# Performance work log

Measured on AMD Instinct MI355X. Metric: run time of the kernel, lower is better.

The kernel has to match this reference:

```python
import jax, jax.numpy as jnp
import numpy as np

TEMPERATURE = 0.07
NEG = -1e9  # stand-in for -inf on the diagonal; exp(NEG) == 0


def setup_inputs() -> dict:
    key = jax.random.key(0)
    k1, k2, k3 = jax.random.split(key, 3)
    B, D = 4096, 1024
    return {
        "anchor_features": jax.random.normal(k1, (B, D), dtype=jnp.float32),
        "positive_features": jax.random.normal(k2, (B, D), dtype=jnp.float32),
        "labels": jax.random.randint(k3, (B,), 0, 2),
    }


def reference(anchor_features, positive_features, labels):
    B = anchor_features.shape[0]
    # L2-normalize (normalize=True)
    a = anchor_features / jnp.linalg.norm(anchor_features, axis=1, keepdims=True)
    p = positive_features / jnp.linalg.norm(positive_features, axis=1, keepdims=True)
    feats = jnp.concatenate([a, p], axis=0)                      # [2B, D]
    sim = jnp.matmul(feats, feats.T) / TEMPERATURE               # [2B, 2B]
    diag = jnp.eye(2 * B, dtype=bool)
    sim = jnp.where(diag, NEG, sim)                              # mask self-similarity
    # logsumexp over all non-self entries per row (diag contributes exp(NEG)=0)
    lse = jax.nn.logsumexp(sim, axis=1)                          # [2B]
    # positive pair similarity: sim[i, i+B] == sim[i+B, i] == <a_i, p_i>/t
    cross = jnp.sum(a * p, axis=1) / TEMPERATURE                 # [B]
    pos_sim = jnp.concatenate([cross, cross])                    # [2B]
    lab = jnp.concatenate([labels, labels]).astype(sim.dtype)    # [2B], 0/1
    per_row = (-pos_sim + lse) * lab
    num_pos = jnp.sum(lab)
    return jnp.where(num_pos > 0, jnp.sum(per_row) / num_pos, jnp.float32(0.0))
```

## Files before the change

kernel.cpp:

```cpp
#include <hip/hip_runtime.h>
#include <hip/hip_bf16.h>

#define TEMP_INV (1.0f / 0.07f)
#define LOG2E 1.4426950408889634f
#define LN2 0.6931471805599453f
#define CFIX 21.0f

typedef __attribute__((ext_vector_type(4))) float f32x4;

__device__ __forceinline__ void gload16(const unsigned char* g,
                                        unsigned char* l) {
  __builtin_amdgcn_global_load_lds(
      (const __attribute__((address_space(1))) void*)g,
      (__attribute__((address_space(3))) void*)l, 16, 0, 0);
}

__global__ __launch_bounds__(256) void norm_kernel(
    const float* __restrict__ A, const float* __restrict__ P,
    unsigned char* __restrict__ F, float* __restrict__ cross,
    float* __restrict__ lsum, int B, int D) {
  const int row = blockIdx.x;
  const int t = threadIdx.x;
  {
    const int zi = row * 256 + t;
    if (zi < 2 * B) lsum[zi] = 0.f;
  }
  const float4* a4 = reinterpret_cast<const float4*>(A + (size_t)row * D);
  const float4* p4 = reinterpret_cast<const float4*>(P + (size_t)row * D);
  const int n4 = D >> 2;
  float sa = 0.f, sp = 0.f, sx = 0.f;
  for (int i = t; i < n4; i += 256) {
    float4 av = a4[i], pv = p4[i];
    sa += av.x * av.x + av.y * av.y + av.z * av.z + av.w * av.w;
    sp += pv.x * pv.x + pv.y * pv.y + pv.z * pv.z + pv.w * pv.w;
    sx += av.x * pv.x + av.y * pv.y + av.z * pv.z + av.w * pv.w;
  }
#pragma unroll
  for (int off = 32; off; off >>= 1) {
    sa += __shfl_down(sa, off);
    sp += __shfl_down(sp, off);
    sx += __shfl_down(sx, off);
  }
  __shared__ float red[3][4];
  const int wid = t >> 6, lane = t & 63;
  if (lane == 0) { red[0][wid] = sa; red[1][wid] = sp; red[2][wid] = sx; }
  __syncthreads();
  sa = red[0][0] + red[0][1] + red[0][2] + red[0][3];
  sp = red[1][0] + red[1][1] + red[1][2] + red[1][3];
  sx = red[2][0] + red[2][1] + red[2][2] + red[2][3];
  const float ian = rsqrtf(sa), ipn = rsqrtf(sp);
  const float ia = ian * 16.f, ip = ipn * 16.f;
  unsigned char* fa = F + (size_t)row * D;
  unsigned char* fp = F + (size_t)(B + row) * D;
  for (int i = t; i < n4; i += 256) {
    float4 av = a4[i], pv = p4[i];
    int qa = 0, qp = 0;
    qa = __builtin_amdgcn_cvt_pk_fp8_f32(av.x * ia, av.y * ia, qa, false);
    qa = __builtin_amdgcn_cvt_pk_fp8_f32(av.z * ia, av.w * ia, qa, true);
    qp = __builtin_amdgcn_cvt_pk_fp8_f32(pv.x * ip, pv.y * ip, qp, false);
    qp = __builtin_amdgcn_cvt_pk_fp8_f32(pv.z * ip, pv.w * ip, qp, true);
    reinterpret_cast<int*>(fa)[i] = qa;
    reinterpret_cast<int*>(fp)[i] = qp;
  }
  if (t == 0) cross[row] = sx * ian * ipn;
}

template <int MFN>
__device__ __forceinline__ void gram_body(
    unsigned char* LDS, const unsigned char* F, float* lsum, int D,
    int r0, int c0, bool diag) {
  const int t = threadIdx.x;
  const int lane = t & 63, w = t >> 6;
  const int lo = lane & 15, hi = lane >> 4;
  const int wr = w >> 2, wn = w & 3;

  const int ciA = t & (MFN * 64 - 1);
  const int lrA = ciA >> 3, cuA = (ciA & 7) ^ (lrA & 7);
  const int trA = lrA * 4 + (cuA >> 1), kcA = (cuA & 1) << 4;
  const int lrB = t >> 3, cuB = (t & 7) ^ (lrB & 7);
  const int trB = lrB * 4 + (cuB >> 1), kcB = (cuB & 1) << 4;
  const unsigned char* sA = F + (size_t)(c0 + trA) * D + kcA;
  const unsigned char* sB = F + (size_t)(r0 + trB) * D + kcB;
  const int dstA = (w % MFN) * 1024;
  const int dstB = w * 1024;

  int offA[MFN], offB[4];
#pragma unroll
  for (int mf = 0; mf < MFN; ++mf) {
    const int r = wr * (MFN * 16) + mf * 16 + lo;
    const int lr = r >> 2;
    const int cu = ((r & 3) << 1) | (hi >> 1);
    offA[mf] = lr * 128 + ((cu ^ (lr & 7)) << 4) + ((hi & 1) << 3);
  }
#pragma unroll
  for (int nf = 0; nf < 4; ++nf) {
    const int r = wn * 64 + nf * 16 + lo;
    const int lr = r >> 2;
    const int cu = ((r & 3) << 1) | (hi >> 1);
    offB[nf] = lr * 128 + ((cu ^ (lr & 7)) << 4) + ((hi & 1) << 3);
  }

#define STAGE(V, KS)                                                       \
  do {                                                                    \
    int v_ = (V); if (v_ > 15) v_ = 15;                                   \
    const int o_ = v_ * 64 + (KS) * 32;                                   \
    gload16(sA + o_, LDS + ((V) & 3) * 32768 + (KS) * 8192 + dstA);       \
    gload16(sB + o_, LDS + ((V) & 3) * 32768 + 16384 + (KS) * 8192 + dstB); \
  } while (0)

  f32x4 acc[MFN][4];
#pragma unroll
  for (int a = 0; a < MFN; ++a)
#pragma unroll
    for (int bb = 0; bb < 4; ++bb) acc[a][bb] = (f32x4){0.f, 0.f, 0.f, 0.f};

  STAGE(0, 0); STAGE(0, 1);
  STAGE(1, 0); STAGE(1, 1);
  STAGE(2, 0); STAGE(2, 1);

  for (int v = 0; v < 16; ++v) {
    const int buf = v & 3;
    asm volatile("s_waitcnt vmcnt(8)" ::: "memory");
    __builtin_amdgcn_s_barrier();
    asm volatile("" ::: "memory");

    const unsigned char* RA0 = LDS + buf * 32768;
    const unsigned char* RA1 = RA0 + 8192;
    const unsigned char* RB0 = LDS + buf * 32768 + 16384;
    const unsigned char* RB1 = RB0 + 8192;
    long a0[MFN], a1[MFN], b0[4], b1[4];
#pragma unroll
    for (int nf = 0; nf < 4; ++nf) b0[nf] = *(const long*)(RB0 + offB[nf]);
#pragma unroll
    for (int mf = 0; mf < MFN; ++mf) a0[mf] = *(const long*)(RA0 + offA[mf]);
#pragma unroll
    for (int nf = 0; nf < 4; ++nf) b1[nf] = *(const long*)(RB1 + offB[nf]);
#pragma unroll
    for (int mf = 0; mf < MFN; ++mf) a1[mf] = *(const long*)(RA1 + offA[mf]);

    STAGE(v + 3, 0);
    STAGE(v + 3, 1);

    __builtin_amdgcn_s_setprio(1);
#pragma unroll
    for (int mf = 0; mf < MFN; ++mf)
#pragma unroll
      for (int nf = 0; nf < 4; ++nf)
        acc[mf][nf] = __builtin_amdgcn_mfma_f32_16x16x32_fp8_fp8(
            a0[mf], b0[nf], acc[mf][nf], 0, 0, 0);
#pragma unroll
    for (int mf = 0; mf < MFN; ++mf)
#pragma unroll
      for (int nf = 0; nf < 4; ++nf)
        acc[mf][nf] = __builtin_amdgcn_mfma_f32_16x16x32_fp8_fp8(
            a1[mf], b1[nf], acc[mf][nf], 0, 0, 0);
    __builtin_amdgcn_s_setprio(0);
    asm volatile("" ::: "memory");
  }

  const float scl = LOG2E * TEMP_INV / 256.f;
  float s_i[4] = {0.f, 0.f, 0.f, 0.f};
  float s_j[MFN * 4];
#pragma unroll
  for (int q = 0; q < MFN * 4; ++q) s_j[q] = 0.f;
  {
    const int jb2 = c0 + wr * (MFN * 16);
#pragma unroll
    for (int nf = 0; nf < 4; ++nf) {
      const int dg = (r0 + wn * 64 + nf * 16 + lo) - jb2;
#pragma unroll
      for (int mf = 0; mf < MFN; ++mf)
#pragma unroll
        for (int rg = 0; rg < 4; ++rg) {
          const int jloc = mf * 16 + hi * 4 + rg;
          float e = exp2f(acc[mf][nf][rg] * scl - CFIX);
          if (diag && dg == jloc) e = 0.f;
          s_i[nf] += e;
          s_j[mf * 4 + rg] += e;
        }
    }
  }
#pragma unroll
  for (int nf = 0; nf < 4; ++nf) {
    float v = s_i[nf];
    v += __shfl_xor(v, 16);
    v += __shfl_xor(v, 32);
    if (hi == 0) atomicAdd(&lsum[r0 + wn * 64 + nf * 16 + lo], v);
  }
  if (!diag) {
#pragma unroll
    for (int q = 0; q < MFN * 4; ++q) {
      float v = s_j[q];
      v += __shfl_xor(v, 1);
      v += __shfl_xor(v, 2);
      v += __shfl_xor(v, 4);
      v += __shfl_xor(v, 8);
      if (lo == 0)
        atomicAdd(&lsum[c0 + wr * (MFN * 16) + (q >> 2) * 16 + hi * 4 +
                        (q & 3)],
                  v);
    }
  }
  asm volatile("s_waitcnt vmcnt(0)" ::: "memory");
#undef STAGE
}

__global__ __launch_bounds__(512, 2) void gram_lse_kernel(
    const unsigned char* __restrict__ F, float* __restrict__ lsum, int NN,
    int D) {
  __shared__ unsigned char lds8[4][2][2][8192];
  const int nrb = NN >> 8;
  const int ntri = nrb * (nrb + 1) / 2;
  const int nfull = ntri - 16;
  const int bidx = blockIdx.x;
  int lin, c0extra = 0;
  bool half = false;
  if (bidx < nfull) {
    lin = bidx;
    if ((nfull & 7) == 0) lin = (bidx & 7) * (nfull >> 3) + (bidx >> 3);
  } else {
    const int idx = bidx - nfull;
    lin = nfull + (idx >> 1);
    c0extra = (idx & 1) * 128;
    half = true;
  }
  int by = (int)((sqrtf(8.f * (float)lin + 1.f) - 1.f) * 0.5f);
  while ((by + 1) * (by + 2) / 2 <= lin) ++by;
  while (by * (by + 1) / 2 > lin) --by;
  const int bx = lin - by * (by + 1) / 2;
  const int r0 = bx * 256;
  const int c0 = by * 256 + c0extra;
  const bool diag = (bx == by);

  if (!half)
    gram_body<8>(&lds8[0][0][0][0], F, lsum, D, r0, c0, diag);
  else
    gram_body<4>(&lds8[0][0][0][0], F, lsum, D, r0, c0, diag);
}

__global__ __launch_bounds__(256) void finalize_part(
    const float* __restrict__ lsum, const float* __restrict__ cross,
    const int* __restrict__ labels, float* __restrict__ bsum,
    float* __restrict__ bcnt, int B) {
  const int NN = 2 * B;
  const int i = blockIdx.x * 256 + threadIdx.x;
  float sum = 0.f, cnt = 0.f;
  if (i < NN) {
    const float lse = LN2 * (CFIX + log2f(lsum[i]));
    const float lab = (float)labels[i % B];
    sum = (lse - cross[i % B] * TEMP_INV) * lab;
    cnt = lab;
  }
#pragma unroll
  for (int off = 32; off; off >>= 1) {
    sum += __shfl_down(sum, off);
    cnt += __shfl_down(cnt, off);
  }
  __shared__ float rs[4], rc[4];
  const int wid = threadIdx.x >> 6, lane = threadIdx.x & 63;
  if (lane == 0) { rs[wid] = sum; rc[wid] = cnt; }
  __syncthreads();
  if (threadIdx.x == 0) {
    bsum[blockIdx.x] = rs[0] + rs[1] + rs[2] + rs[3];
    bcnt[blockIdx.x] = rc[0] + rc[1] + rc[2] + rc[3];
  }
}

__global__ __launch_bounds__(64) void finalize_final(
    const float* __restrict__ bsum, const float* __restrict__ bcnt,
    float* __restrict__ out, int nb) {
  const int t = threadIdx.x;
  float s = (t < nb) ? bsum[t] : 0.f;
  float c = (t < nb) ? bcnt[t] : 0.f;
#pragma unroll
  for (int off = 32; off; off >>= 1) {
    s += __shfl_down(s, off);
    c += __shfl_down(c, off);
  }
  if (t == 0) out[0] = (c > 0.f) ? s / c : 0.f;
}

extern "C" void kernel_launch(void* const* d_in, const int* in_sizes, int n_in,
                              void* d_out, int out_size, void* d_ws, size_t ws_size,
                              hipStream_t stream) {
  const float* A = (const float*)d_in[0];
  const float* P = (const float*)d_in[1];
  const int* labels = (const int*)d_in[2];
  float* out = (float*)d_out;
  const int B = in_sizes[2];
  const int D = in_sizes[0] / B;
  const int NN = 2 * B;

  char* ws = (char*)d_ws;
  unsigned char* F = (unsigned char*)ws;
  size_t off = (size_t)NN * D;
  off = (off + 255) & ~(size_t)255;
  float* cross = (float*)(ws + off);
  off += (size_t)B * sizeof(float);
  off = (off + 255) & ~(size_t)255;
  float* lsum = (float*)(ws + off);
  off += (size_t)NN * sizeof(float);
  off = (off + 255) & ~(size_t)255;
  float* bsum = (float*)(ws + off);
  off += 64 * sizeof(float);
  float* bcnt = (float*)(ws + off);

  norm_kernel<<<B, 256, 0, stream>>>(A, P, F, cross, lsum, B, D);
  const int nrb = NN >> 8;
  const int ntri = nrb * (nrb + 1) / 2;
  const int nblk = (ntri - 16) + 32;
  gram_lse_kernel<<<nblk, 512, 0, stream>>>(F, lsum, NN, D);
  const int nb = (NN + 255) / 256;
  finalize_part<<<nb, 256, 0, stream>>>(lsum, cross, labels, bsum, bcnt, B);
  finalize_final<<<1, 64, 0, stream>>>(bsum, bcnt, out, nb);
}
```

Baseline: 116.1 us.

## Restructure full-tile gram loop into fine-grained 8-phase double-buffered pipeline

```diff
diff --git a/kernel.cpp b/kernel.cpp
--- a/kernel.cpp
+++ b/kernel.cpp
@@ -65,10 +65,156 @@
   if (t == 0) cross[row] = sx * ian * ipn;
 }
 
-template <int MFN>
-__device__ __forceinline__ void gram_body(
+
+__device__ __forceinline__ void gram_full8(
     unsigned char* LDS, const unsigned char* F, float* lsum, int D,
     int r0, int c0, bool diag) {
+  const int t = threadIdx.x;
+  const int lane = t & 63, w = t >> 6;
+  const int lo = lane & 15, hi = lane >> 4;
+  const int wr = w >> 2, wn = w & 3;
+
+  const int lineS = t >> 3, cS = (t & 7) ^ (lineS & 7);
+  const int trS = lineS * 4 + (cS >> 1), kcS = (cS & 1) << 4;
+  const unsigned char* sA = F + (size_t)(c0 + trS) * D + kcS;
+  const unsigned char* sB = F + (size_t)(r0 + trS) * D + kcS;
+  const int dstW = w * 1024;
+
+  int offA[8], offB[4];
+#pragma unroll
+  for (int mf = 0; mf < 8; ++mf) {
+    const int r = wr * 128 + mf * 16 + lo;
+    const int lr = r >> 2;
+    const int cu = ((r & 3) << 1) | (hi >> 1);
+    offA[mf] = lr * 128 + ((cu ^ (lr & 7)) << 4) + ((hi & 1) << 3);
+  }
+#pragma unroll
+  for (int nf = 0; nf < 4; ++nf) {
+    const int r = wn * 64 + nf * 16 + lo;
+    const int lr = r >> 2;
+    const int cu = ((r & 3) << 1) | (hi >> 1);
+    offB[nf] = lr * 128 + ((cu ^ (lr & 7)) << 4) + ((hi & 1) << 3);
+  }
+
+#define STAGE_A(T, KS, BUF)                                                 \
+  do {                                                                      \
+    int v_ = (T); if (v_ > 15) v_ = 15;                                     \
+    gload16(sA + v_ * 64 + (KS) * 32,                                       \
+            LDS + (BUF) * 32768 + (KS) * 8192 + dstW);                      \
+  } while (0)
+#define STAGE_B(T, KS, BUF)                                                 \
+  do {                                                                      \
+    int v_ = (T); if (v_ > 15) v_ = 15;                                     \
+    gload16(sB + v_ * 64 + (KS) * 32,                                       \
+            LDS + (BUF) * 32768 + 16384 + (KS) * 8192 + dstW);              \
+  } while (0)
+
+  f32x4 acc[8][4];
+  long bfr[4];
+
+#define PHASE(BUF, MH, KS, READB, STAGE_STMT, WAIT2)                          \
+  do {                                                                        \
+    const unsigned char* RA_ = LDS + (BUF) * 32768 + (KS) * 8192;             \
+    const unsigned char* RB_ = RA_ + 16384;                                   \
+    if (READB) {                                                              \
+      _Pragma("unroll") for (int nf = 0; nf < 4; ++nf)                        \
+          bfr[nf] = *(const long*)(RB_ + offB[nf]);                           \
+    }                                                                         \
+    long af[4];                                                               \
+    _Pragma("unroll") for (int m = 0; m < 4; ++m)                             \
+        af[m] = *(const long*)(RA_ + offA[(MH)*4 + m]);                       \
+    STAGE_STMT;                                                               \
+    if (WAIT2) asm volatile("s_waitcnt vmcnt(2)" ::: "memory");               \
+    asm volatile("" ::: "memory");                                            \
+    __builtin_amdgcn_s_barrier();                                             \
+    asm volatile("" ::: "memory");                                            \
+    __builtin_amdgcn_s_setprio(1);                                            \
+    _Pragma("unroll") for (int m = 0; m < 4; ++m)                             \
+      _Pragma("unroll") for (int nf = 0; nf < 4; ++nf)                        \
+          acc[(MH)*4 + m][nf] = __builtin_amdgcn_mfma_f32_16x16x32_fp8_fp8(   \
+              af[m], bfr[nf], acc[(MH)*4 + m][nf], 0, 0, 0);                  \
+    __builtin_amdgcn_s_setprio(0);                                            \
+    asm volatile("" ::: "memory");                                            \
+    __builtin_amdgcn_s_barrier();                                             \
+    asm volatile("" ::: "memory");                                            \
+  } while (0)
+
+#pragma unroll
+  for (int a = 0; a < 8; ++a)
+#pragma unroll
+    for (int bb = 0; bb < 4; ++bb) acc[a][bb] = (f32x4){0.f, 0.f, 0.f, 0.f};
+
+  STAGE_A(0, 0, 0); STAGE_B(0, 0, 0);
+  STAGE_A(0, 1, 0); STAGE_B(0, 1, 0);
+  STAGE_A(1, 0, 1); STAGE_B(1, 0, 1);
+  STAGE_B(1, 1, 1);
+  asm volatile("s_waitcnt vmcnt(3)" ::: "memory");
+  __builtin_amdgcn_s_barrier();
+  asm volatile("" ::: "memory");
+
+  for (int it = 0; it < 8; ++it) {
+    const int tt = it * 2;
+    PHASE(0, 0, 0, true,  STAGE_A(tt + 1, 1, 1), false);
+    PHASE(0, 1, 0, false, STAGE_B(tt + 2, 0, 0), false);
+    PHASE(0, 0, 1, true,  STAGE_A(tt + 2, 0, 0), false);
+    PHASE(0, 1, 1, false, STAGE_B(tt + 2, 1, 0), true);
+    PHASE(1, 0, 0, true,  STAGE_A(tt + 2, 1, 0), false);
+    PHASE(1, 1, 0, false, STAGE_B(tt + 3, 0, 1), false);
+    PHASE(1, 0, 1, true,  STAGE_A(tt + 3, 0, 1), false);
+    PHASE(1, 1, 1, false, STAGE_B(tt + 3, 1, 1), true);
+  }
+
+  const float scl = LOG2E * TEMP_INV / 256.f;
+  float s_i[4] = {0.f, 0.f, 0.f, 0.f};
+  float s_j[32];
+#pragma unroll
+  for (int q = 0; q < 32; ++q) s_j[q] = 0.f;
+  {
+    const int jb2 = c0 + wr * 128;
+#pragma unroll
+    for (int nf = 0; nf < 4; ++nf) {
+      const int dg = (r0 + wn * 64 + nf * 16 + lo) - jb2;
+#pragma unroll
+      for (int mf = 0; mf < 8; ++mf)
+#pragma unroll
+        for (int rg = 0; rg < 4; ++rg) {
+          const int jloc = mf * 16 + hi * 4 + rg;
+          float e = exp2f(acc[mf][nf][rg] * scl - CFIX);
+          if (diag && dg == jloc) e = 0.f;
+          s_i[nf] += e;
+          s_j[mf * 4 + rg] += e;
+        }
+    }
+  }
+#pragma unroll
+  for (int nf = 0; nf < 4; ++nf) {
+    float v = s_i[nf];
+    v += __shfl_xor(v, 16);
+    v += __shfl_xor(v, 32);
+    if (hi == 0) atomicAdd(&lsum[r0 + wn * 64 + nf * 16 + lo], v);
+  }
+  if (!diag) {
+#pragma unroll
+    for (int q = 0; q < 32; ++q) {
+      float v = s_j[q];
+      v += __shfl_xor(v, 1);
+      v += __shfl_xor(v, 2);
+      v += __shfl_xor(v, 4);
+      v += __shfl_xor(v, 8);
+      if (lo == 0)
+        atomicAdd(&lsum[c0 + wr * 128 + (q >> 2) * 16 + hi * 4 + (q & 3)], v);
+    }
+  }
+  asm volatile("s_waitcnt vmcnt(0)" ::: "memory");
+#undef PHASE
+#undef STAGE_A
+#undef STAGE_B
+}
+
+__device__ __forceinline__ void gram_half(
+    unsigned char* LDS, const unsigned char* F, float* lsum, int D,
+    int r0, int c0, bool diag) {
+  const int MFN = 4;
   const int t = threadIdx.x;
   const int lane = t & 63, w = t >> 6;
   const int lo = lane & 15, hi = lane >> 4;
@@ -100,11 +246,11 @@
     offB[nf] = lr * 128 + ((cu ^ (lr & 7)) << 4) + ((hi & 1) << 3);
   }
 
-#define STAGE(V, KS)                                                       \
-  do {                                                                    \
-    int v_ = (V); if (v_ > 15) v_ = 15;                                   \
-    const int o_ = v_ * 64 + (KS) * 32;                                   \
-    gload16(sA + o_, LDS + ((V) & 3) * 32768 + (KS) * 8192 + dstA);       \
+#define STAGE(V, KS)                                                        \
+  do {                                                                      \
+    int v_ = (V); if (v_ > 15) v_ = 15;                                     \
+    const int o_ = v_ * 64 + (KS) * 32;                                     \
+    gload16(sA + o_, LDS + ((V) & 3) * 32768 + (KS) * 8192 + dstA);         \
     gload16(sB + o_, LDS + ((V) & 3) * 32768 + 16384 + (KS) * 8192 + dstB); \
   } while (0)
 
@@ -126,7 +272,7 @@
 
     const unsigned char* RA0 = LDS + buf * 32768;
     const unsigned char* RA1 = RA0 + 8192;
-    const unsigned char* RB0 = LDS + buf * 32768 + 16384;
+    const unsigned char* RB0 = RA0 + 16384;
     const unsigned char* RB1 = RB0 + 8192;
     long a0[MFN], a1[MFN], b0[4], b1[4];
 #pragma unroll
@@ -208,7 +354,7 @@
 __global__ __launch_bounds__(512, 2) void gram_lse_kernel(
     const unsigned char* __restrict__ F, float* __restrict__ lsum, int NN,
     int D) {
-  __shared__ unsigned char lds8[4][2][2][8192];
+  __shared__ unsigned char lds8[4][32768];
   const int nrb = NN >> 8;
   const int ntri = nrb * (nrb + 1) / 2;
   const int nfull = ntri - 16;
@@ -233,9 +379,9 @@
   const bool diag = (bx == by);
 
   if (!half)
-    gram_body<8>(&lds8[0][0][0][0], F, lsum, D, r0, c0, diag);
+    gram_full8(&lds8[0][0], F, lsum, D, r0, c0, diag);
   else
-    gram_body<4>(&lds8[0][0][0][0], F, lsum, D, r0, c0, diag);
+    gram_half(&lds8[0][0], F, lsum, D, r0, c0, diag);
 }
 
 __global__ __launch_bounds__(256) void finalize_part(
```

Result: no change. 115.8 us (-0.2%).

## Split gram kernel into 1024-thread full-tile kernel and separate half-tile kernel

Applied to the files above, without the earlier changes.

```diff
diff --git a/kernel.cpp b/kernel.cpp
--- a/kernel.cpp
+++ b/kernel.cpp
@@ -65,10 +65,162 @@
   if (t == 0) cross[row] = sx * ian * ipn;
 }
 
-template <int MFN>
-__device__ __forceinline__ void gram_body(
-    unsigned char* LDS, const unsigned char* F, float* lsum, int D,
-    int r0, int c0, bool diag) {
+
+__global__ __launch_bounds__(1024) void gram_full_kernel(
+    const unsigned char* __restrict__ F, float* __restrict__ lsum, int NN,
+    int D) {
+  __shared__ unsigned char lds8[4][2][2][8192];
+  int lin = blockIdx.x;
+  lin = (lin & 7) * 64 + (lin >> 3);
+  int by = (int)((sqrtf(8.f * (float)lin + 1.f) - 1.f) * 0.5f);
+  while ((by + 1) * (by + 2) / 2 <= lin) ++by;
+  while (by * (by + 1) / 2 > lin) --by;
+  const int bx = lin - by * (by + 1) / 2;
+  const int r0 = bx * 256;
+  const int c0 = by * 256;
+  const bool diag = (bx == by);
+
+  const int t = threadIdx.x;
+  const int lane = t & 63, w = t >> 6;
+  const int lo = lane & 15, hi = lane >> 4;
+  const int wr = w >> 2, wn = w & 3;
+
+  const int KSa = t >> 9;
+  const int cS = t & 511;
+  const int lineS = cS >> 3, pS = (cS & 7) ^ (lineS & 7);
+  const int trS = lineS * 4 + (pS >> 1);
+  const int kcS = ((pS & 1) << 4) + KSa * 32;
+  const unsigned char* sA = F + (size_t)(c0 + trS) * D + kcS;
+  const unsigned char* sB = F + (size_t)(r0 + trS) * D + kcS;
+  const int dstW = (w & 7) * 1024;
+
+  int offA[4], offB[4];
+#pragma unroll
+  for (int mf = 0; mf < 4; ++mf) {
+    const int r = wr * 64 + mf * 16 + lo;
+    const int lr = r >> 2;
+    const int cu = ((r & 3) << 1) | (hi >> 1);
+    offA[mf] = lr * 128 + ((cu ^ (lr & 7)) << 4) + ((hi & 1) << 3);
+  }
+#pragma unroll
+  for (int nf = 0; nf < 4; ++nf) {
+    const int r = wn * 64 + nf * 16 + lo;
+    const int lr = r >> 2;
+    const int cu = ((r & 3) << 1) | (hi >> 1);
+    offB[nf] = lr * 128 + ((cu ^ (lr & 7)) << 4) + ((hi & 1) << 3);
+  }
+
+#define STAGE(V)                                                      \
+  do {                                                                \
+    int v_ = (V); if (v_ > 15) v_ = 15;                               \
+    gload16(sA + v_ * 64, &lds8[(V) & 3][0][KSa][dstW]);              \
+    gload16(sB + v_ * 64, &lds8[(V) & 3][1][KSa][dstW]);              \
+  } while (0)
+
+  f32x4 acc[4][4];
+#pragma unroll
+  for (int a = 0; a < 4; ++a)
+#pragma unroll
+    for (int bb = 0; bb < 4; ++bb) acc[a][bb] = (f32x4){0.f, 0.f, 0.f, 0.f};
+
+  STAGE(0); STAGE(1); STAGE(2);
+
+  for (int v = 0; v < 16; ++v) {
+    const int buf = v & 3;
+    asm volatile("s_waitcnt vmcnt(4)" ::: "memory");
+    __builtin_amdgcn_s_barrier();
+    asm volatile("" ::: "memory");
+
+    long a0[4], a1[4], b0[4], b1[4];
+#pragma unroll
+    for (int q = 0; q < 4; ++q) {
+      b0[q] = *(const long*)(&lds8[buf][1][0][0] + offB[q]);
+      a0[q] = *(const long*)(&lds8[buf][0][0][0] + offA[q]);
+      b1[q] = *(const long*)(&lds8[buf][1][1][0] + offB[q]);
+      a1[q] = *(const long*)(&lds8[buf][0][1][0] + offA[q]);
+    }
+
+    STAGE(v + 3);
+
+    __builtin_amdgcn_s_setprio(1);
+#pragma unroll
+    for (int mf = 0; mf < 4; ++mf)
+#pragma unroll
+      for (int nf = 0; nf < 4; ++nf)
+        acc[mf][nf] = __builtin_amdgcn_mfma_f32_16x16x32_fp8_fp8(
+            a0[mf], b0[nf], acc[mf][nf], 0, 0, 0);
+#pragma unroll
+    for (int mf = 0; mf < 4; ++mf)
+#pragma unroll
+      for (int nf = 0; nf < 4; ++nf)
+        acc[mf][nf] = __builtin_amdgcn_mfma_f32_16x16x32_fp8_fp8(
+            a1[mf], b1[nf], acc[mf][nf], 0, 0, 0);
+    __builtin_amdgcn_s_setprio(0);
+    asm volatile("" ::: "memory");
+  }
+
+  const float scl = LOG2E * TEMP_INV / 256.f;
+  float s_i[4] = {0.f, 0.f, 0.f, 0.f};
+  float s_j[16];
+#pragma unroll
+  for (int q = 0; q < 16; ++q) s_j[q] = 0.f;
+  {
+    const int dgb = (r0 + wn * 64) - (c0 + wr * 64);
+#pragma unroll
+    for (int nf = 0; nf < 4; ++nf) {
+      const int dg = dgb + nf * 16 + lo;
+#pragma unroll
+      for (int mf = 0; mf < 4; ++mf)
+#pragma unroll
+        for (int rg = 0; rg < 4; ++rg) {
+          const int jloc = mf * 16 + hi * 4 + rg;
+          float e = exp2f(acc[mf][nf][rg] * scl - CFIX);
+          if (diag && dg == jloc) e = 0.f;
+          s_i[nf] += e;
+          s_j[mf * 4 + rg] += e;
+        }
+    }
+  }
+#pragma unroll
+  for (int nf = 0; nf < 4; ++nf) {
+    float v = s_i[nf];
+    v += __shfl_xor(v, 16);
+    v += __shfl_xor(v, 32);
+    if (hi == 0) atomicAdd(&lsum[r0 + wn * 64 + nf * 16 + lo], v);
+  }
+  if (!diag) {
+#pragma unroll
+    for (int q = 0; q < 16; ++q) {
+      float v = s_j[q];
+      v += __shfl_xor(v, 1);
+      v += __shfl_xor(v, 2);
+      v += __shfl_xor(v, 4);
+      v += __shfl_xor(v, 8);
+      if (lo == 0)
+        atomicAdd(&lsum[c0 + wr * 64 + (q >> 2) * 16 + hi * 4 + (q & 3)], v);
+    }
+  }
+  asm volatile("s_waitcnt vmcnt(0)" ::: "memory");
+#undef STAGE
+}
+
+__global__ __launch_bounds__(512, 2) void gram_half_kernel(
+    const unsigned char* __restrict__ F, float* __restrict__ lsum, int NN,
+    int D) {
+  __shared__ unsigned char LDSb[4][32768];
+  unsigned char* LDS = &LDSb[0][0];
+  const int MFN = 4;
+  const int idx = blockIdx.x;
+  const int lin = 512 + (idx >> 1);
+  const int c0extra = (idx & 1) * 128;
+  int by = (int)((sqrtf(8.f * (float)lin + 1.f) - 1.f) * 0.5f);
+  while ((by + 1) * (by + 2) / 2 <= lin) ++by;
+  while (by * (by + 1) / 2 > lin) --by;
+  const int bx = lin - by * (by + 1) / 2;
+  const int r0 = bx * 256;
+  const int c0 = by * 256 + c0extra;
+  const bool diag = (bx == by);
+
   const int t = threadIdx.x;
   const int lane = t & 63, w = t >> 6;
   const int lo = lane & 15, hi = lane >> 4;
@@ -100,11 +252,11 @@
     offB[nf] = lr * 128 + ((cu ^ (lr & 7)) << 4) + ((hi & 1) << 3);
   }
 
-#define STAGE(V, KS)                                                       \
-  do {                                                                    \
-    int v_ = (V); if (v_ > 15) v_ = 15;                                   \
-    const int o_ = v_ * 64 + (KS) * 32;                                   \
-    gload16(sA + o_, LDS + ((V) & 3) * 32768 + (KS) * 8192 + dstA);       \
+#define STAGE(V, KS)                                                        \
+  do {                                                                      \
+    int v_ = (V); if (v_ > 15) v_ = 15;                                     \
+    const int o_ = v_ * 64 + (KS) * 32;                                     \
+    gload16(sA + o_, LDS + ((V) & 3) * 32768 + (KS) * 8192 + dstA);         \
     gload16(sB + o_, LDS + ((V) & 3) * 32768 + 16384 + (KS) * 8192 + dstB); \
   } while (0)
 
@@ -126,7 +278,7 @@
 
     const unsigned char* RA0 = LDS + buf * 32768;
     const unsigned char* RA1 = RA0 + 8192;
-    const unsigned char* RB0 = LDS + buf * 32768 + 16384;
+    const unsigned char* RB0 = RA0 + 16384;
     const unsigned char* RB1 = RB0 + 8192;
     long a0[MFN], a1[MFN], b0[4], b1[4];
 #pragma unroll
@@ -203,39 +355,6 @@
   }
   asm volatile("s_waitcnt vmcnt(0)" ::: "memory");
 #undef STAGE
-}
-
-__global__ __launch_bounds__(512, 2) void gram_lse_kernel(
-    const unsigned char* __restrict__ F, float* __restrict__ lsum, int NN,
-    int D) {
-  __shared__ unsigned char lds8[4][2][2][8192];
-  const int nrb = NN >> 8;
-  const int ntri = nrb * (nrb + 1) / 2;
-  const int nfull = ntri - 16;
-  const int bidx = blockIdx.x;
-  int lin, c0extra = 0;
-  bool half = false;
-  if (bidx < nfull) {
-    lin = bidx;
-    if ((nfull & 7) == 0) lin = (bidx & 7) * (nfull >> 3) + (bidx >> 3);
-  } else {
-    const int idx = bidx - nfull;
-    lin = nfull + (idx >> 1);
-    c0extra = (idx & 1) * 128;
-    half = true;
-  }
-  int by = (int)((sqrtf(8.f * (float)lin + 1.f) - 1.f) * 0.5f);
-  while ((by + 1) * (by + 2) / 2 <= lin) ++by;
-  while (by * (by + 1) / 2 > lin) --by;
-  const int bx = lin - by * (by + 1) / 2;
-  const int r0 = bx * 256;
-  const int c0 = by * 256 + c0extra;
-  const bool diag = (bx == by);
-
-  if (!half)
-    gram_body<8>(&lds8[0][0][0][0], F, lsum, D, r0, c0, diag);
-  else
-    gram_body<4>(&lds8[0][0][0][0], F, lsum, D, r0, c0, diag);
 }
 
 __global__ __launch_bounds__(256) void finalize_part(
@@ -306,10 +425,8 @@
   float* bcnt = (float*)(ws + off);
 
   norm_kernel<<<B, 256, 0, stream>>>(A, P, F, cross, lsum, B, D);
-  const int nrb = NN >> 8;
-  const int ntri = nrb * (nrb + 1) / 2;
-  const int nblk = (ntri - 16) + 32;
-  gram_lse_kernel<<<nblk, 512, 0, stream>>>(F, lsum, NN, D);
+  gram_full_kernel<<<512, 1024, 0, stream>>>(F, lsum, NN, D);
+  gram_half_kernel<<<32, 512, 0, stream>>>(F, lsum, NN, D);
   const int nb = (NN + 255) / 256;
   finalize_part<<<nb, 256, 0, stream>>>(lsum, cross, labels, bsum, bcnt, B);
   finalize_final<<<1, 64, 0, stream>>>(bsum, bcnt, out, nb);
```

Result: no change. 115.9 us (-0.2%).
